# Kernel tuning notes

Hardware: AMD Instinct MI355X
Metric: run time of the kernel (lower is better)

The kernel has to match this reference:

```python
import jax, jax.numpy as jnp
import numpy as np

ALPHA = 0.2          # LeakyReLU negative slope
NEG_INF = -9e15      # mask value used by the original module


def setup_inputs() -> dict:
    key = jax.random.key(0)
    k1, k2, k3, k4 = jax.random.split(key, 4)
    N, Din, Dout = 8192, 512, 256
    features = jax.random.normal(k1, (N, Din), dtype=jnp.float32)
    adj = jax.random.randint(k2, (N, N), 0, 2, dtype=jnp.int32)
    W = jax.random.normal(k3, (Din, Dout), dtype=jnp.float32) * (1.414 / np.sqrt(Din))
    a = jax.random.normal(k4, (2 * Dout, 1), dtype=jnp.float32) * (1.414 / np.sqrt(2 * Dout))
    return {"features": features, "adj": adj, "W": W, "a": a}


def reference(features, adj, W, a):
    Dout = W.shape[1]
    Wh = features @ W                       # [N, Dout]
    # e_ij = leakyrelu([Wh_i || Wh_j] @ a) decomposes additively:
    # identical math to the N*N*2D concat in the original, without materializing it.
    src = Wh @ a[:Dout, 0]                  # [N]  contribution of node i
    dst = Wh @ a[Dout:, 0]                  # [N]  contribution of node j
    e = jax.nn.leaky_relu(src[:, None] + dst[None, :], negative_slope=ALPHA)  # [N, N]
    masked = jnp.where(adj > 0, e, NEG_INF)
    attention = jax.nn.softmax(masked, axis=1)   # dropout p=0.0 (eval) -> identity
    h_prime = attention @ Wh                # [N, Dout]
    return jax.nn.elu(h_prime)
```

## Files before the change

### kernel.cpp

```cpp
#include <hip/hip_runtime.h>
#include <hip/hip_bf16.h>

#define NN   8192
#define DIN  512
#define DOUT 256

typedef __attribute__((ext_vector_type(8)))  short s16x8;
typedef __attribute__((ext_vector_type(16))) float f32x16;

static __device__ __forceinline__ unsigned short f2bf(float f) {
    union { float f; unsigned u; } v; v.f = f;
    unsigned r = v.u + 0x7fffu + ((v.u >> 16) & 1u);
    return (unsigned short)(r >> 16);
}

static __device__ __forceinline__ void gload_lds16(const void* g, void* l) {
    __builtin_amdgcn_global_load_lds(
        (const __attribute__((address_space(1))) unsigned int*)g,
        (__attribute__((address_space(3))) unsigned int*)l, 16, 0, 0);
}

__global__ __launch_bounds__(256) void k_wh2(const float* __restrict__ feat,
                                             const float* __restrict__ W,
                                             const float* __restrict__ a,
                                             unsigned short* __restrict__ WhT,
                                             float* __restrict__ src,
                                             float* __restrict__ dst) {
    __shared__ float lf[16 * DIN];
    __shared__ float red[2][4][16];
    const int tid = threadIdx.x;
    const int i0  = blockIdx.x * 16;
    const int w   = tid >> 6, lane = tid & 63;

    const float4* fsrc = (const float4*)(feat + (size_t)i0 * DIN);
    float4* fdst = (float4*)lf;
    #pragma unroll
    for (int q = 0; q < 8; ++q) fdst[tid + q * 256] = fsrc[tid + q * 256];
    __syncthreads();

    const int c = tid;
    float outs[16];
    #pragma unroll
    for (int r = 0; r < 16; ++r) outs[r] = 0.f;

    for (int k = 0; k < DIN; k += 4) {
        float w0 = W[(k + 0) * DOUT + c];
        float w1 = W[(k + 1) * DOUT + c];
        float w2 = W[(k + 2) * DOUT + c];
        float w3 = W[(k + 3) * DOUT + c];
        #pragma unroll
        for (int r = 0; r < 16; ++r) {
            float4 f = *(const float4*)&lf[r * DIN + k];
            outs[r] = fmaf(f.x, w0, fmaf(f.y, w1, fmaf(f.z, w2, fmaf(f.w, w3, outs[r]))));
        }
    }

    unsigned short tb[16];
    #pragma unroll
    for (int r = 0; r < 16; ++r) tb[r] = f2bf(outs[r]);
    uint4* wt = (uint4*)(WhT + (size_t)c * NN + i0);
    wt[0] = *(uint4*)&tb[0];
    wt[1] = *(uint4*)&tb[8];

    const float as_ = a[c], ad_ = a[DOUT + c];
    #pragma unroll
    for (int r = 0; r < 16; ++r) {
        float s = outs[r] * as_;
        float d = outs[r] * ad_;
        #pragma unroll
        for (int off = 32; off; off >>= 1) {
            s += __shfl_xor(s, off);
            d += __shfl_xor(d, off);
        }
        if (lane == 0) { red[0][w][r] = s; red[1][w][r] = d; }
    }
    __syncthreads();
    if (tid < 16)
        src[i0 + tid] = red[0][0][tid] + red[0][1][tid] + red[0][2][tid] + red[0][3][tid];
    else if (tid < 32) {
        int r = tid - 16;
        dst[i0 + r] = red[1][0][r] + red[1][1][r] + red[1][2][r] + red[1][3][r];
    }
}


#define STEP_BODY(T, CUR, A0, A1, NA0, NA1)                                              \
{                                                                                        \
                       \
    {                                                                                    \
        const int tn_ = ((T) < 31) ? (T) + 1 : 31;        \
        NA0 = *(const int4*)(adjR + tn_ * 64);                                           \
        NA1 = *(const int4*)(adjR + tn_ * 64 + 4);                                       \
    }                                                                                    \
    {                                                                                    \
        float4 d0_ = *(const float4*)(dstp + (T) * 64);                                  \
        float4 d1_ = *(const float4*)(dstp + (T) * 64 + 4);                              \
        const float dd_[8] = {d0_.x, d0_.y, d0_.z, d0_.w, d1_.x, d1_.y, d1_.z, d1_.w};   \
        const int   va_[8] = {A0.x, A0.y, A0.z, A0.w, A1.x, A1.y, A1.z, A1.w};           \
        s16x8 pw_;                                                                       \
        _Pragma("unroll")                                                                \
        for (int jj = 0; jj < 8; ++jj) {                                                 \
            float x_ = si + dd_[jj];                                                     \
            x_ = fmaxf(x_, 0.2f * x_);                               \
            float p_ = va_[jj] > 0 ? __expf(x_) : 0.f;  \
            den += p_;                                                                   \
            pw_[jj] = (short)f2bf(p_);                                                   \
        }                                                                                \
        *(s16x8*)(Pl[CUR] + pbyte) = pw_;                                                \
    }                                                                                    \
    __builtin_amdgcn_sched_barrier(0);                                                   \
    asm volatile("s_waitcnt vmcnt(2) lgkmcnt(0)" ::: "memory");                          \
    __builtin_amdgcn_s_barrier();                                                        \
    __builtin_amdgcn_sched_barrier(0);                                                   \
            \
    {                                                                                    \
        const int tn_ = ((T) < 31) ? (T) + 1 : 31;                                       \
        const size_t gkb_ = (size_t)(kb0 + tn_ * 64) * 2;                                \
        _Pragma("unroll")                                                                \
        for (int q = 0; q < 4; ++q)                                                      \
            gload_lds16((const char*)WhT + (size_t)colB[q] * (NN * 2) + gkb_ + kbB[q],   \
                        Bs[(CUR) ^ 1] + (q * 512 + tid) * 16);                           \
    }                                                                                    \
    _Pragma("unroll")                                                                    \
    for (int ks4 = 0; ks4 < 4; ++ks4) {                                                  \
        const int kbyte_ = ks4 * 32 + lhi * 16;                                          \
        const int colg_  = c0w + l31;                                                    \
        s16x8 bfv_ = *(const s16x8*)(Bs[CUR] + colg_ * 128 +                             \
                                     (kbyte_ ^ ((colg_ & 7) << 4)));                     \
        _Pragma("unroll")                                                                \
        for (int mt = 0; mt < 2; ++mt) {                                                 \
            const int row_ = mt * 32 + l31;                                              \
            s16x8 afv_ = *(const s16x8*)(Pl[CUR] + row_ * 128 +                          \
                                         (kbyte_ ^ ((row_ & 7) << 4)));                  \
            acc[mt] = __builtin_amdgcn_mfma_f32_32x32x16_bf16(afv_, bfv_, acc[mt], 0, 0, 0); \
        }                                                                                \
    }                                                                                    \
}

__global__ __launch_bounds__(512, 4) void k_attn4(const int* __restrict__ adj,
                                                  const unsigned short* __restrict__ WhT,
                                                  const float* __restrict__ src,
                                                  const float* __restrict__ dstg,
                                                  float* __restrict__ denp,
                                                  float* __restrict__ part) {
    __shared__ __attribute__((aligned(16))) char Bs[2][32768];
    __shared__ __attribute__((aligned(16))) char Pl[2][8192];

    const int tid  = threadIdx.x;
    const int lane = tid & 63;
    const int w    = tid >> 6;
    const int l31  = lane & 31, lhi = lane >> 5;
    const int c0w  = w * 32;

    const int rt  = blockIdx.x & 127;
    const int ks  = blockIdx.x >> 7;
    const int kb0 = ks * 2048;

    const int r  = tid >> 3, kb = tid & 7;
    const int gr = rt * 64 + r;
    const float si = src[gr];
    const int*   adjR = adj  + (size_t)gr * NN + kb0 + kb * 8;
    const float* dstp = dstg +                   kb0 + kb * 8;
    const int pbyte = r * 128 + ((kb * 16) ^ ((r & 7) << 4));

    int colB[4], kbB[4];
    #pragma unroll
    for (int q = 0; q < 4; ++q) {
        int chunk = q * 512 + tid;
        colB[q] = chunk >> 3;
        kbB[q]  = ((chunk & 7) * 16) ^ ((colB[q] & 7) << 4);
    }

    f32x16 acc[2];
    #pragma unroll
    for (int mt = 0; mt < 2; ++mt)
        #pragma unroll
        for (int e = 0; e < 16; ++e) acc[mt][e] = 0.f;
    float den = 0.f;

    #pragma unroll
    for (int q = 0; q < 4; ++q)
        gload_lds16((const char*)WhT + (size_t)colB[q] * (NN * 2) + (size_t)kb0 * 2 + kbB[q],
                    Bs[0] + (q * 512 + tid) * 16);
    int4 a0 = *(const int4*)(adjR);
    int4 a1 = *(const int4*)(adjR + 4);
    int4 n0, n1;

    for (int tt = 0; tt < 16; ++tt) {
        STEP_BODY(2 * tt,     0, a0, a1, n0, n1);
        STEP_BODY(2 * tt + 1, 1, n0, n1, a0, a1);
    }

    den += __shfl_xor(den, 1);
    den += __shfl_xor(den, 2);
    den += __shfl_xor(den, 4);
    if ((tid & 7) == 0) denp[(size_t)ks * NN + gr] = den;

    float* pp = part + (size_t)ks * (NN * DOUT);
    #pragma unroll
    for (int mt = 0; mt < 2; ++mt) {
        #pragma unroll
        for (int e = 0; e < 16; ++e) {
            const int row = rt * 64 + mt * 32 + (e & 3) + 8 * (e >> 2) + 4 * lhi;
            pp[(size_t)row * DOUT + c0w + l31] = acc[mt][e];
        }
    }
}

__global__ __launch_bounds__(256) void k_finish2(const float* __restrict__ part,
                                                 const float* __restrict__ denp,
                                                 float* __restrict__ out) {
    const int idx = blockIdx.x * 256 + threadIdx.x;
    const int row = idx >> 6;
    float den = denp[row] + denp[NN + row] + denp[2 * NN + row] + denp[3 * NN + row];
    float rv = den > 0.f ? 1.f / den : 0.f;
    const int st = NN * DOUT / 4;
    const float4* p = (const float4*)part;
    float4 va = p[idx], vb = p[idx + st], vc = p[idx + 2 * st], vd = p[idx + 3 * st];
    float4 s;
    s.x = (va.x + vb.x + vc.x + vd.x) * rv;
    s.y = (va.y + vb.y + vc.y + vd.y) * rv;
    s.z = (va.z + vb.z + vc.z + vd.z) * rv;
    s.w = (va.w + vb.w + vc.w + vd.w) * rv;
    s.x = s.x > 0.f ? s.x : expm1f(s.x);
    s.y = s.y > 0.f ? s.y : expm1f(s.y);
    s.z = s.z > 0.f ? s.z : expm1f(s.z);
    s.w = s.w > 0.f ? s.w : expm1f(s.w);
    ((float4*)out)[idx] = s;
}

extern "C" void kernel_launch(void* const* d_in, const int* in_sizes, int n_in,
                              void* d_out, int out_size, void* d_ws, size_t ws_size,
                              hipStream_t stream) {
    const float* feat = (const float*)d_in[0];
    const int*   adj  = (const int*)d_in[1];
    const float* W    = (const float*)d_in[2];
    const float* a    = (const float*)d_in[3];
    float* out = (float*)d_out;

    char* ws = (char*)d_ws;
    unsigned short* WhT  = (unsigned short*)ws;
    float*          src  = (float*)(ws + 4194304);
    float*          dst  = (float*)(ws + 4227072);
    float*          denp = (float*)(ws + 4259840);
    float*          part = (float*)(ws + 4390912);

    k_wh2    <<<512,  256, 0, stream>>>(feat, W, a, WhT, src, dst);
    k_attn4  <<<512,  512, 0, stream>>>(adj, WhT, src, dst, denp, part);
    k_finish2<<<2048, 256, 0, stream>>>(part, denp, out);
}
```

Before: 180.3 us.

## Pack adjacency into bitmask in projection kernel and software-pipeline attention P-tile

The projection kernel now also streams the int32 adjacency matrix and packs it into a byte-per-8-entries bitmask laid out for the attention kernel. The attention kernel reads these bits instead of the full int32 adj, and it computes the next step's probability tile after the current MFMAs so the exp work overlaps the WhT prefetch. This cuts the attention kernel's traffic but still reads adj once in full and adds a write and read of an 8 MB bitmask. The barrier now waits on vmcnt(0) instead of vmcnt(2).

```diff
diff --git a/kernel.cpp b/kernel.cpp
--- a/kernel.cpp
+++ b/kernel.cpp
@@ -20,12 +20,14 @@
         (__attribute__((address_space(3))) unsigned int*)l, 16, 0, 0);
 }
 
-__global__ __launch_bounds__(256) void k_wh2(const float* __restrict__ feat,
+__global__ __launch_bounds__(256) void k_whm(const float* __restrict__ feat,
                                              const float* __restrict__ W,
                                              const float* __restrict__ a,
+                                             const int* __restrict__ adj,
                                              unsigned short* __restrict__ WhT,
                                              float* __restrict__ src,
-                                             float* __restrict__ dst) {
+                                             float* __restrict__ dst,
+                                             unsigned char* __restrict__ bits) {
     __shared__ float lf[16 * DIN];
     __shared__ float red[2][4][16];
     const int tid = threadIdx.x;
@@ -81,39 +83,26 @@
         int r = tid - 16;
         dst[i0 + r] = red[1][0][r] + red[1][1][r] + red[1][2][r] + red[1][3][r];
     }
-}
-
-
-#define STEP_BODY(T, CUR, A0, A1, NA0, NA1)                                              \
+
+    const size_t gbase = (size_t)blockIdx.x * 256 + tid;
+    for (int it = 0; it < 64; ++it) {
+        const size_t g = gbase + (size_t)it * 131072;
+        const int row = (int)(g >> 10);
+        const int b   = (int)(g & 1023);
+        const int s_  = b >> 8, t_ = (b >> 3) & 31, kb_ = b & 7;
+        const int4 v0 = *(const int4*)(adj + g * 8);
+        const int4 v1 = *(const int4*)(adj + g * 8 + 4);
+        unsigned int m = (v0.x > 0 ? 1u : 0u) | (v0.y > 0 ? 2u : 0u) |
+                         (v0.z > 0 ? 4u : 0u) | (v0.w > 0 ? 8u : 0u) |
+                         (v1.x > 0 ? 16u : 0u) | (v1.y > 0 ? 32u : 0u) |
+                         (v1.z > 0 ? 64u : 0u) | (v1.w > 0 ? 128u : 0u);
+        bits[(size_t)row * 1024 + s_ * 256 + kb_ * 32 + t_] = (unsigned char)m;
+    }
+}
+
+#define STEP5(T, CUR)                                                                    \
 {                                                                                        \
-                       \
-    {                                                                                    \
-        const int tn_ = ((T) < 31) ? (T) + 1 : 31;        \
-        NA0 = *(const int4*)(adjR + tn_ * 64);                                           \
-        NA1 = *(const int4*)(adjR + tn_ * 64 + 4);                                       \
-    }                                                                                    \
-    {                                                                                    \
-        float4 d0_ = *(const float4*)(dstp + (T) * 64);                                  \
-        float4 d1_ = *(const float4*)(dstp + (T) * 64 + 4);                              \
-        const float dd_[8] = {d0_.x, d0_.y, d0_.z, d0_.w, d1_.x, d1_.y, d1_.z, d1_.w};   \
-        const int   va_[8] = {A0.x, A0.y, A0.z, A0.w, A1.x, A1.y, A1.z, A1.w};           \
-        s16x8 pw_;                                                                       \
-        _Pragma("unroll")                                                                \
-        for (int jj = 0; jj < 8; ++jj) {                                                 \
-            float x_ = si + dd_[jj];                                                     \
-            x_ = fmaxf(x_, 0.2f * x_);                               \
-            float p_ = va_[jj] > 0 ? __expf(x_) : 0.f;  \
-            den += p_;                                                                   \
-            pw_[jj] = (short)f2bf(p_);                                                   \
-        }                                                                                \
-        *(s16x8*)(Pl[CUR] + pbyte) = pw_;                                                \
-    }                                                                                    \
-    __builtin_amdgcn_sched_barrier(0);                                                   \
-    asm volatile("s_waitcnt vmcnt(2) lgkmcnt(0)" ::: "memory");                          \
-    __builtin_amdgcn_s_barrier();                                                        \
-    __builtin_amdgcn_sched_barrier(0);                                                   \
-            \
-    {                                                                                    \
+    {                   \
         const int tn_ = ((T) < 31) ? (T) + 1 : 31;                                       \
         const size_t gkb_ = (size_t)(kb0 + tn_ * 64) * 2;                                \
         _Pragma("unroll")                                                                \
@@ -121,6 +110,7 @@
             gload_lds16((const char*)WhT + (size_t)colB[q] * (NN * 2) + gkb_ + kbB[q],   \
                         Bs[(CUR) ^ 1] + (q * 512 + tid) * 16);                           \
     }                                                                                    \
+                                                     \
     _Pragma("unroll")                                                                    \
     for (int ks4 = 0; ks4 < 4; ++ks4) {                                                  \
         const int kbyte_ = ks4 * 32 + lhi * 16;                                          \
@@ -135,9 +125,27 @@
             acc[mt] = __builtin_amdgcn_mfma_f32_32x32x16_bf16(afv_, bfv_, acc[mt], 0, 0, 0); \
         }                                                                                \
     }                                                                                    \
-}
-
-__global__ __launch_bounds__(512, 4) void k_attn4(const int* __restrict__ adj,
+    if ((T) < 31) {                                       \
+        const unsigned int m8_ = browp[(T) + 1];                                         \
+        float4 d0_ = *(const float4*)(dstp + ((T) + 1) * 64);                            \
+        float4 d1_ = *(const float4*)(dstp + ((T) + 1) * 64 + 4);                        \
+        const float dd_[8] = {d0_.x, d0_.y, d0_.z, d0_.w, d1_.x, d1_.y, d1_.z, d1_.w};   \
+        s16x8 pw_;                                                                       \
+        _Pragma("unroll")                                                                \
+        for (int jj = 0; jj < 8; ++jj) {                                                 \
+            float x_ = si + dd_[jj];                                                     \
+            x_ = fmaxf(x_, 0.2f * x_);                               \
+            float p_ = (m8_ >> jj) & 1u ? __expf(x_) : 0.f;     \
+            den += p_;                                                                   \
+            pw_[jj] = (short)f2bf(p_);                                                   \
+        }                                                                                \
+        *(s16x8*)(Pl[(CUR) ^ 1] + pbyte) = pw_;                                          \
+    }                                                                                    \
+    asm volatile("s_waitcnt vmcnt(0) lgkmcnt(0)" ::: "memory");                          \
+    __builtin_amdgcn_s_barrier();                                                        \
+}
+
+__global__ __launch_bounds__(512, 4) void k_attn5(const unsigned char* __restrict__ bits,
                                                   const unsigned short* __restrict__ WhT,
                                                   const float* __restrict__ src,
                                                   const float* __restrict__ dstg,
@@ -159,8 +167,8 @@
     const int r  = tid >> 3, kb = tid & 7;
     const int gr = rt * 64 + r;
     const float si = src[gr];
-    const int*   adjR = adj  + (size_t)gr * NN + kb0 + kb * 8;
-    const float* dstp = dstg +                   kb0 + kb * 8;
+    const unsigned char* browp = bits + (size_t)gr * 1024 + ks * 256 + kb * 32;
+    const float* dstp = dstg + kb0 + kb * 8;
     const int pbyte = r * 128 + ((kb * 16) ^ ((r & 7) << 4));
 
     int colB[4], kbB[4];
@@ -182,13 +190,28 @@
     for (int q = 0; q < 4; ++q)
         gload_lds16((const char*)WhT + (size_t)colB[q] * (NN * 2) + (size_t)kb0 * 2 + kbB[q],
                     Bs[0] + (q * 512 + tid) * 16);
-    int4 a0 = *(const int4*)(adjR);
-    int4 a1 = *(const int4*)(adjR + 4);
-    int4 n0, n1;
+    {
+        const unsigned int m8 = browp[0];
+        float4 d0 = *(const float4*)(dstp);
+        float4 d1 = *(const float4*)(dstp + 4);
+        const float dd[8] = {d0.x, d0.y, d0.z, d0.w, d1.x, d1.y, d1.z, d1.w};
+        s16x8 pw;
+        #pragma unroll
+        for (int jj = 0; jj < 8; ++jj) {
+            float x = si + dd[jj];
+            x = fmaxf(x, 0.2f * x);
+            float p = (m8 >> jj) & 1u ? __expf(x) : 0.f;
+            den += p;
+            pw[jj] = (short)f2bf(p);
+        }
+        *(s16x8*)(Pl[0] + pbyte) = pw;
+    }
+    asm volatile("s_waitcnt vmcnt(0) lgkmcnt(0)" ::: "memory");
+    __builtin_amdgcn_s_barrier();
 
     for (int tt = 0; tt < 16; ++tt) {
-        STEP_BODY(2 * tt,     0, a0, a1, n0, n1);
-        STEP_BODY(2 * tt + 1, 1, n0, n1, a0, a1);
+        STEP5(2 * tt,     0);
+        STEP5(2 * tt + 1, 1);
     }
 
     den += __shfl_xor(den, 1);
@@ -243,9 +266,10 @@
     float*          src  = (float*)(ws + 4194304);
     float*          dst  = (float*)(ws + 4227072);
     float*          denp = (float*)(ws + 4259840);
-    float*          part = (float*)(ws + 4390912);
-
-    k_wh2    <<<512,  256, 0, stream>>>(feat, W, a, WhT, src, dst);
-    k_attn4  <<<512,  512, 0, stream>>>(adj, WhT, src, dst, denp, part);
+    unsigned char*  bits = (unsigned char*)(ws + 4390912);
+    float*          part = (float*)(ws + 12779520);
+
+    k_whm    <<<512,  256, 0, stream>>>(feat, W, a, adj, WhT, src, dst, bits);
+    k_attn5  <<<512,  512, 0, stream>>>(bits, WhT, src, dst, denp, part);
     k_finish2<<<2048, 256, 0, stream>>>(part, denp, out);
 }
```

Result: slower. 192.7 us (+6.9%).
